# Optimization experiments

Hardware: AMD Instinct MI355X
Metric: run time of the kernel (lower is better)

Reference implementation:

```python
import jax, jax.numpy as jnp
import numpy as np

PS = 5    # patch_w for rgb arch
K = 14    # num nearest neighbors
WS = 29   # search window side


def _patchify(img_pad, H, W):
    """img_pad: [t, H+2*(whalf+phalf), W+..., c] channels-last.
    Returns patch features over the search grid: [t, H+2*whalf, W+2*whalf, PS*PS*c]."""
    whalf = WS // 2
    Hg, Wg = H + 2 * whalf, W + 2 * whalf
    slices = [img_pad[:, dy:dy + Hg, dx:dx + Wg, :]
              for dy in range(PS) for dx in range(PS)]
    return jnp.concatenate(slices, axis=-1)


def _forward(noisy, sigma):
    t, c, H, W = noisy.shape
    # rescale to [-1,1] and remove per-frame channel means (as in forward)
    x = (noisy / 255.0 - 0.5) / 0.5
    means = x.mean((-2, -1), keepdims=True)
    x = x - means
    xl = jnp.transpose(x, (0, 2, 3, 1))  # [t,H,W,c]

    phalf, whalf = PS // 2, WS // 2
    pad = phalf + whalf
    xp = jnp.pad(xl, ((0, 0), (pad, pad), (pad, pad), (0, 0)), mode='reflect')

    P = _patchify(xp, H, W)              # [t, H+2*whalf, W+2*whalf, D]
    D = PS * PS * c
    Pq = P[:, whalf:whalf + H, whalf:whalf + W, :]  # query patches [t,H,W,D]

    # --- windowed kNN patch search: scan over WS*WS offsets ---
    def dist_step(_, o):
        oy, ox = o // WS, o % WS
        Pn = jax.lax.dynamic_slice(P, (0, oy, ox, 0), (t, H, W, D))
        d = jnp.sum((Pq - Pn) ** 2, axis=-1)  # [t,H,W]
        return None, d

    _, dists = jax.lax.scan(dist_step, None, jnp.arange(WS * WS))
    dists = jnp.transpose(dists, (1, 2, 3, 0))  # [t,H,W,WS*WS]

    negv, idx = jax.lax.top_k(-dists, K)        # k smallest distances
    dk = -negv                                   # [t,H,W,K]
    oy, ox = idx // WS, idx % WS

    # --- gather neighbor patches ---
    rows = jnp.arange(H)[None, :, None, None] + oy   # [t,H,W,K]
    cols = jnp.arange(W)[None, None, :, None] + ox
    ti = jnp.arange(t)[:, None, None, None]
    neigh = P[ti, rows, cols]                        # [t,H,W,K,D]

    # --- patch denoise: distance-softmax weighted neighbor aggregation ---
    sig = (jnp.float32(sigma) / 255.0) / 0.5
    beta = 1.0 / (2.0 * sig * sig * D)
    wts = jax.nn.softmax(-beta * dk, axis=-1)        # [t,H,W,K]
    pdeno = jnp.einsum('thwk,thwkd->thwd', wts, neigh)  # [t,H,W,D]
    patches = pdeno.reshape(t, H, W, PS, PS, c)

    # --- weighted iFold: overlap-add + count normalization ---
    acc = jnp.zeros((t, H + 2 * phalf, W + 2 * phalf, c), x.dtype)
    cnt = jnp.zeros((t, H + 2 * phalf, W + 2 * phalf, 1), x.dtype)
    ones = jnp.ones((t, H, W, 1), x.dtype)
    for py in range(PS):
        for px in range(PS):
            acc = acc.at[:, py:py + H, px:px + W, :].add(patches[:, :, :, py, px, :])
            cnt = cnt.at[:, py:py + H, px:px + W, :].add(ones)
    deno = acc / cnt
    deno = deno[:, phalf:H + phalf, phalf:W + phalf, :]  # final_format crop

    deno = jnp.transpose(deno, (0, 3, 1, 2)) + means
    deno = 255.0 * (deno * 0.5 + 0.5)
    return deno


def setup_inputs() -> dict:
    key = jax.random.key(0)
    k1, _ = jax.random.split(key)
    noisy = jax.random.uniform(k1, (4, 3, 128, 128), dtype=jnp.float32) * 255.0
    sigma = 25
    return {"noisy": noisy, "sigma": sigma}


def reference(noisy, sigma):
    return _forward(noisy, sigma)
```

## Files before the change

### kernel.cpp

```cpp
#include <hip/hip_runtime.h>

#define T_ 4
#define H_ 128
#define W_ 128
#define XPS 160
#define WSZ 29
#define K_ 14
#define ACCS 132

#define SROWS 4
#define SCOLS 12
#define TR 36
#define TC 44
#define NBI 32
#define NBJ 11
#define NW 4
#define OPW 211

#define DPP_SHL(x, n) __uint_as_float((unsigned)__builtin_amdgcn_update_dpp( \
        0, (int)__float_as_uint(x), 0x100 + (n), 0xF, 0xF, true))

__global__ void k_means(const float* __restrict__ noisy, float* __restrict__ means) {
    int tc = blockIdx.x;
    const float* src = noisy + (size_t)tc * (H_ * W_);
    float s = 0.f;
    for (int i = threadIdx.x; i < H_ * W_; i += 256) s += src[i];
    __shared__ float red[256];
    red[threadIdx.x] = s;
    __syncthreads();
    for (int st = 128; st > 0; st >>= 1) {
        if ((int)threadIdx.x < st) red[threadIdx.x] += red[threadIdx.x + st];
        __syncthreads();
    }
    if (threadIdx.x == 0)
        means[tc] = red[0] * (1.f / (H_ * W_)) * (2.f / 255.f) - 1.f;
}

__global__ void k_pad(const float* __restrict__ noisy, const float* __restrict__ means,
                      float* __restrict__ xp) {
    int idx = blockIdx.x * 256 + threadIdx.x;
    if (idx >= T_ * XPS * XPS) return;
    int t  = idx / (XPS * XPS);
    int rr = (idx / XPS) % XPS;
    int cc = idx % XPS;
    int ry = rr - 16; if (ry < 0) ry = -ry; if (ry > H_ - 1) ry = 2 * (H_ - 1) - ry;
    int rx = cc - 16; if (rx < 0) rx = -rx; if (rx > W_ - 1) rx = 2 * (W_ - 1) - rx;
    float* dst = xp + (size_t)idx * 3;
#pragma unroll
    for (int c = 0; c < 3; c++) {
        float v = noisy[(((size_t)t * 3 + c) * H_ + ry) * W_ + rx];
        dst[c] = v * (2.f / 255.f) - 1.f - means[t * 3 + c];
    }
}

__global__ __launch_bounds__(256, 4)
void k_main(const float* __restrict__ xp, const int* __restrict__ sigma_p,
            float* __restrict__ acc) {
    __shared__ __align__(16) float tile[TR][TC][3];
    __shared__ unsigned kbuf[NW * K_][49];

    const int tid = threadIdx.x;
    const int b   = blockIdx.x;
    const int t   = b / (NBI * NBJ);
    const int rem = b % (NBI * NBJ);
    const int bi  = (rem / NBJ) * SROWS;
    const int bj  = (rem % NBJ) * SCOLS;

    const float* src = xp + ((size_t)(t * XPS + bi) * XPS + bj) * 3;
    for (int i = tid; i < TR * 33; i += 256) {
        int rr = i / 33, q = i - rr * 33;
        float4 v = *reinterpret_cast<const float4*>(src + (size_t)rr * (XPS * 3) + q * 4);
        *reinterpret_cast<float4*>(&tile[rr][0][0] + q * 4) = v;
    }
    __syncthreads();

    const int w    = tid >> 6;
    const int lane = tid & 63;
    const int g    = lane >> 4;
    const int tj   = lane & 15;
    const bool valid = (tj < SCOLS) && (bj + tj < W_);

    float A[5][3];
#pragma unroll
    for (int dy = 0; dy < 5; dy++)
#pragma unroll
        for (int c = 0; c < 3; c++)
            A[dy][c] = tile[14 + g + dy][14 + tj][c];

    unsigned keys[K_];
#pragma unroll
    for (int k = 0; k < K_; k++) keys[k] = 0xFFFFFF00u + k;
    unsigned kmax = 0xFFFFFF00u + (K_ - 1);

    const int o0 = w * OPW;
    const int on = (o0 + OPW <= WSZ * WSZ) ? OPW : (WSZ * WSZ - o0);
    for (int i = 0; i < on; i++) {
        int o  = o0 + i;
        int oy = o / WSZ;
        int ox = o - oy * WSZ;
        const float* bp = &tile[g + oy][tj + ox][0];
        float cs = 0.f;
#pragma unroll
        for (int dy = 0; dy < 5; dy++) {
            float d0 = A[dy][0] - bp[dy * (TC * 3) + 0];
            float d1 = A[dy][1] - bp[dy * (TC * 3) + 1];
            float d2 = A[dy][2] - bp[dy * (TC * 3) + 2];
            cs = cs + d0 * d0 + d1 * d1 + d2 * d2;
        }
        float D = cs;
        D += DPP_SHL(cs, 1);
        D += DPP_SHL(cs, 2);
        D += DPP_SHL(cs, 3);
        D += DPP_SHL(cs, 4);
        unsigned key = (__float_as_uint(D) & 0xFFFFFC00u) | (unsigned)o;
        if (valid && key < kmax) {
#pragma unroll
            for (int k = 0; k < K_; k++) keys[k] = (keys[k] == kmax) ? key : keys[k];
            kmax = keys[0];
#pragma unroll
            for (int k = 1; k < K_; k++) kmax = keys[k] > kmax ? keys[k] : kmax;
        }
    }

    const int pxi = g * SCOLS + tj;
    if (valid) {
#pragma unroll
        for (int k = 0; k < K_; k++) kbuf[w * K_ + k][pxi] = keys[k];
    }
#pragma unroll
    for (int k = 0; k < K_; k++) keys[k] = 0xFFFFFF00u + k;
    kmax = 0xFFFFFF00u + (K_ - 1);
    __syncthreads();

    if (valid) {
        for (int j = 0; j < NW * K_; j++) {
            unsigned key = kbuf[j][pxi];
            if (key < kmax) {
#pragma unroll
                for (int k = 0; k < K_; k++) keys[k] = (keys[k] == kmax) ? key : keys[k];
                kmax = keys[0];
#pragma unroll
                for (int k = 1; k < K_; k++) kmax = keys[k] > kmax ? keys[k] : kmax;
            }
        }
    }

    float sig  = (float)sigma_p[0] * (2.f / 255.f);
    float beta = 1.f / (2.f * sig * sig * 75.f);
    float wk[K_];
    int oyk[K_], oxk[K_];
    float dmin = 3.4e38f;
#pragma unroll
    for (int k = 0; k < K_; k++) {
        float dv = __uint_as_float(keys[k] & 0xFFFFFC00u);
        wk[k] = dv;
        int ok = (int)(keys[k] & 1023u);
        oyk[k] = ok / WSZ;
        oxk[k] = ok - oyk[k] * WSZ;
        dmin = fminf(dmin, dv);
    }
    float sw = 0.f;
#pragma unroll
    for (int k = 0; k < K_; k++) { float e = __expf(beta * (dmin - wk[k])); wk[k] = e; sw += e; }
    float inv = 1.f / sw;
#pragma unroll
    for (int k = 0; k < K_; k++) wk[k] *= inv;

    __syncthreads();
    float* accb = reinterpret_cast<float*>(&kbuf[0][0]);
    for (int i = tid; i < 8 * 16 * 3; i += 256) accb[i] = 0.f;
    __syncthreads();

    for (int p = w; p < 25; p += NW) {
        int py = p / 5, px = p - py * 5;
        if (valid) {
            float s0 = 0.f, s1 = 0.f, s2 = 0.f;
#pragma unroll
            for (int k = 0; k < K_; k++) {
                const float* nb = &tile[g + oyk[k] + py][tj + oxk[k] + px][0];
                s0 += wk[k] * nb[0];
                s1 += wk[k] * nb[1];
                s2 += wk[k] * nb[2];
            }
            float* ap = accb + ((g + py) * 16 + (tj + px)) * 3;
            atomicAdd(ap + 0, s0);
            atomicAdd(ap + 1, s1);
            atomicAdd(ap + 2, s2);
        }
    }
    __syncthreads();

    for (int i = tid; i < 8 * 16 * 3; i += 256) {
        int ch = i % 3;
        int cc = (i / 3) & 15;
        int rr = i / 48;
        int gr = bi + rr, gc = bj + cc;
        if (gc < ACCS)
            atomicAdd(&acc[(((size_t)t * ACCS + gr) * ACCS + gc) * 3 + ch], accb[i]);
    }
}

__global__ void k_final(const float* __restrict__ acc, const float* __restrict__ means,
                        float* __restrict__ out) {
    int idx = blockIdx.x * 256 + threadIdx.x;
    if (idx >= T_ * 3 * H_ * W_) return;
    int j  = idx & 127;
    int i  = (idx >> 7) & 127;
    int ch = (idx >> 14) % 3;
    int t  = idx / (3 * H_ * W_);
    int r = i + 2, s = j + 2;
    int ny = (r < 4 ? r : 4) - (r > 127 ? r - 127 : 0) + 1;
    int nx = (s < 4 ? s : 4) - (s > 127 ? s - 127 : 0) + 1;
    float v = acc[(((size_t)t * ACCS + r) * ACCS + s) * 3 + ch] / (float)(ny * nx);
    v += means[t * 3 + ch];
    out[idx] = 127.5f * v + 127.5f;
}

extern "C" void kernel_launch(void* const* d_in, const int* in_sizes, int n_in,
                              void* d_out, int out_size, void* d_ws, size_t ws_size,
                              hipStream_t stream) {
    (void)in_sizes; (void)n_in; (void)out_size; (void)ws_size;
    const float* noisy = (const float*)d_in[0];
    const int*   sigma = (const int*)d_in[1];

    float* means = (float*)d_ws;
    float* xp    = means + 64;
    float* acc   = xp + (size_t)T_ * XPS * XPS * 3;
    float* out   = (float*)d_out;

    hipLaunchKernelGGL(k_means, dim3(12), dim3(256), 0, stream, noisy, means);
    hipLaunchKernelGGL(k_pad, dim3((T_ * XPS * XPS + 255) / 256), dim3(256), 0, stream,
                       noisy, means, xp);
    hipMemsetAsync(acc, 0, (size_t)T_ * ACCS * ACCS * 3 * sizeof(float), stream);
    hipLaunchKernelGGL(k_main, dim3(T_ * NBI * NBJ), dim3(256), 0, stream, xp, sigma, acc);
    hipLaunchKernelGGL(k_final, dim3((T_ * 3 * H_ * W_ + 255) / 256), dim3(256), 0, stream,
                       acc, means, out);
}
```

Before: 303.7 us.

## Compute patch distances via norm expansion with precomputed patch norms

Replaces the squared-difference distance with ||q||^2 + ||n||^2 - 2<q,n>, precomputing all 5x5 patch squared norms in shared memory through a separable row-then-column sum. The inner loop becomes pure FMAs instead of subtract-multiply-add, and the tile row stride is padded to 136 floats, likely to change LDS bank mapping. The expansion can lose precision through cancellation, which is clamped at zero but may alter neighbor ordering. It also adds extra shared memory, two preprocessing passes and an extra barrier.

```diff
diff --git a/kernel.cpp b/kernel.cpp
--- a/kernel.cpp
+++ b/kernel.cpp
@@ -12,10 +12,14 @@
 #define SCOLS 12
 #define TR 36
 #define TC 44
+#define RS 136
 #define NBI 32
 #define NBJ 11
 #define NW 4
 #define OPW 211
+
+#define HS 40
+#define N2S 48
 
 #define DPP_SHL(x, n) __uint_as_float((unsigned)__builtin_amdgcn_update_dpp( \
         0, (int)__float_as_uint(x), 0x100 + (n), 0xF, 0xF, true))
@@ -56,8 +60,9 @@
 __global__ __launch_bounds__(256, 4)
 void k_main(const float* __restrict__ xp, const int* __restrict__ sigma_p,
             float* __restrict__ acc) {
-    __shared__ __align__(16) float tile[TR][TC][3];
+    __shared__ __align__(16) float tileF[TR * RS];
     __shared__ unsigned kbuf[NW * K_][49];
+    __shared__ float N2s[32 * N2S];
 
     const int tid = threadIdx.x;
     const int b   = blockIdx.x;
@@ -70,7 +75,25 @@
     for (int i = tid; i < TR * 33; i += 256) {
         int rr = i / 33, q = i - rr * 33;
         float4 v = *reinterpret_cast<const float4*>(src + (size_t)rr * (XPS * 3) + q * 4);
-        *reinterpret_cast<float4*>(&tile[rr][0][0] + q * 4) = v;
+        *reinterpret_cast<float4*>(&tileF[rr * RS + q * 4]) = v;
+    }
+    __syncthreads();
+
+    float* hbuf = reinterpret_cast<float*>(&kbuf[0][0]);
+    for (int i = tid; i < TR * HS; i += 256) {
+        int r = i / HS, c = i - (i / HS) * HS;
+        const float* tp = &tileF[r * RS + c * 3];
+        float s = 0.f;
+#pragma unroll
+        for (int d = 0; d < 15; d++) { float v = tp[d]; s = fmaf(v, v, s); }
+        hbuf[i] = s;
+    }
+    __syncthreads();
+
+    for (int i = tid; i < 32 * HS; i += 256) {
+        int r = i / HS, c = i - (i / HS) * HS;
+        const float* hp = &hbuf[r * HS + c];
+        N2s[r * N2S + c] = hp[0] + hp[HS] + hp[2 * HS] + hp[3 * HS] + hp[4 * HS];
     }
     __syncthreads();
 
@@ -85,7 +108,8 @@
     for (int dy = 0; dy < 5; dy++)
 #pragma unroll
         for (int c = 0; c < 3; c++)
-            A[dy][c] = tile[14 + g + dy][14 + tj][c];
+            A[dy][c] = tileF[(14 + g + dy) * RS + (14 + tj) * 3 + c];
+    const float N2q = N2s[(g + 14) * N2S + (tj + 14)];
 
     unsigned keys[K_];
 #pragma unroll
@@ -98,20 +122,21 @@
         int o  = o0 + i;
         int oy = o / WSZ;
         int ox = o - oy * WSZ;
-        const float* bp = &tile[g + oy][tj + ox][0];
-        float cs = 0.f;
+        const float* bp = &tileF[(g + oy) * RS + (tj + ox) * 3];
+        float cb = 0.f;
 #pragma unroll
         for (int dy = 0; dy < 5; dy++) {
-            float d0 = A[dy][0] - bp[dy * (TC * 3) + 0];
-            float d1 = A[dy][1] - bp[dy * (TC * 3) + 1];
-            float d2 = A[dy][2] - bp[dy * (TC * 3) + 2];
-            cs = cs + d0 * d0 + d1 * d1 + d2 * d2;
-        }
-        float D = cs;
-        D += DPP_SHL(cs, 1);
-        D += DPP_SHL(cs, 2);
-        D += DPP_SHL(cs, 3);
-        D += DPP_SHL(cs, 4);
+            cb = fmaf(A[dy][0], bp[dy * RS + 0], cb);
+            cb = fmaf(A[dy][1], bp[dy * RS + 1], cb);
+            cb = fmaf(A[dy][2], bp[dy * RS + 2], cb);
+        }
+        float CB = cb;
+        CB += DPP_SHL(cb, 1);
+        CB += DPP_SHL(cb, 2);
+        CB += DPP_SHL(cb, 3);
+        CB += DPP_SHL(cb, 4);
+        float D = fmaf(-2.f, CB, N2q + N2s[(g + oy) * N2S + (tj + ox)]);
+        D = fmaxf(D, 0.f);
         unsigned key = (__float_as_uint(D) & 0xFFFFFC00u) | (unsigned)o;
         if (valid && key < kmax) {
 #pragma unroll
@@ -122,6 +147,7 @@
         }
     }
 
+    __syncthreads();
     const int pxi = g * SCOLS + tj;
     if (valid) {
 #pragma unroll
@@ -177,7 +203,7 @@
             float s0 = 0.f, s1 = 0.f, s2 = 0.f;
 #pragma unroll
             for (int k = 0; k < K_; k++) {
-                const float* nb = &tile[g + oyk[k] + py][tj + oxk[k] + px][0];
+                const float* nb = &tileF[(g + oyk[k] + py) * RS + (tj + oxk[k] + px) * 3];
                 s0 += wk[k] * nb[0];
                 s1 += wk[k] * nb[1];
                 s2 += wk[k] * nb[2];
```

Measured after the change: 305.0 us. No clear change (+0.4%).
